# Optimization experiments

Measured on AMD Instinct MI355X. Metric: run time of the kernel, lower is better.

The kernel has to match this reference:

```python
import jax, jax.numpy as jnp
import numpy as np

B, XDIM, TWIN, INCH = 1024, 62, 10, 128
MID, OUT, K, K1, LIN, HC = 256, 512, 3, 10, 512, 4
EPS = 1e-5

REGIONS = [
    list(range(0, 5)),
    list(range(5, 8)) + list(range(14, 17)),
    list(range(8, 11)) + list(range(17, 20)),
    list(range(11, 14)) + list(range(20, 23)),
    list(range(23, 26)) + list(range(32, 35)),
    list(range(26, 29)) + list(range(35, 38)),
    list(range(29, 32)) + list(range(38, 41)),
    list(range(41, 44)) + list(range(50, 52)) + list(range(57, 58)),
    list(range(44, 47)) + list(range(52, 55)) + list(range(58, 61)),
    list(range(47, 50)) + list(range(55, 57)) + list(range(61, 62)),
]


def setup_inputs() -> dict:
    key = jax.random.key(0)
    ks = jax.random.split(key, 40)
    n = lambda k, s, sc=0.02: jax.random.normal(k, s, jnp.float32) * sc
    inp = {
        "x": jax.random.normal(ks[0], (B, XDIM, TWIN, INCH), jnp.float32),
        "tfe_w": n(ks[1], (XDIM, TWIN)),          # depthwise Conv2d (10,1) weight, squeezed
        "tfe_b": jnp.zeros((XDIM,), jnp.float32),
        "cheby1_w": n(ks[2], (K, INCH, OUT)),
        "A": n(ks[3], (XDIM, XDIM)),
        "cheby2_w": n(ks[4], (K, MID, OUT)),
        "A1": n(ks[5], (K1, K1)),
        "b_gate": jnp.float32(1.0),
        "c_gate": jnp.float32(1.0),
        "region_b": jnp.zeros((K1, MID), jnp.float32),
        "hc_w1": n(ks[6], (OUT * 72, LIN)),
        "hc_b1": jnp.zeros((LIN,), jnp.float32),
        "bn1_g": jnp.ones((LIN,), jnp.float32),
        "bn1_b": jnp.zeros((LIN,), jnp.float32),
        "hc_w2": n(ks[7], (LIN, LIN // 2)),
        "hc_b2": jnp.zeros((LIN // 2,), jnp.float32),
        "bn2_g": jnp.ones((LIN // 2,), jnp.float32),
        "bn2_b": jnp.zeros((LIN // 2,), jnp.float32),
        "hc_w3": n(ks[8], (LIN // 2, HC)),
        "hc_b3": jnp.zeros((HC,), jnp.float32),
    }
    for i, idx in enumerate(REGIONS):
        inp[f"rw{i+1}"] = n(ks[10 + i], (MID, INCH, len(idx)))
    return inp


def _cheby(x, L, Ws):
    # sum_k  S_k @ x @ W_k  with S_0 = I, S_k = S_{k-1} @ L ; then ReLU
    S = jnp.eye(L.shape[0], dtype=x.dtype)
    res = jnp.zeros(x.shape[:2] + (Ws.shape[-1],), x.dtype)
    for k in range(Ws.shape[0]):
        res = res + jnp.einsum("nm,bmt,to->bno", S, x, Ws[k])
        S = S @ L
    return jax.nn.relu(res)


def _bn(h, g, b):
    mu = h.mean(axis=0)
    v = h.var(axis=0)  # biased, training-mode BatchNorm1d
    return (h - mu) * jax.lax.rsqrt(v + EPS) * g + b


def _forward(x, tfe_w, tfe_b, cheby1_w, A, cheby2_w, A1, b_gate, c_gate,
             rw1, rw2, rw3, rw4, rw5, rw6, rw7, rw8, rw9, rw10, region_b,
             hc_w1, hc_b1, bn1_g, bn1_b, hc_w2, hc_b2, bn2_g, bn2_b, hc_w3, hc_b3):
    # variance gate (torch.var default: unbiased)
    sigma = jnp.var(x, axis=2, ddof=1)                              # (B, 62, INCH)
    g_tfe = jnp.einsum("bcit,ci->bct", x, tfe_w) + tfe_b[None, :, None]
    g = g_tfe * jnp.exp(-sigma)                                      # (B, 62, INCH)

    g1 = _cheby(g, A, cheby1_w)                                      # (B, 62, OUT)

    rws = [rw1, rw2, rw3, rw4, rw5, rw6, rw7, rw8, rw9, rw10]
    RG = []
    for i, (idx, w) in enumerate(zip(REGIONS, rws)):
        reg = g[:, jnp.asarray(idx), :]                              # (B, L, INCH)
        RG.append(jnp.einsum("blc,mcl->bm", reg, w) + region_b[i])   # Conv1d, full-width kernel
    g2in = jnp.stack(RG, axis=1)                                     # (B, 10, MID)
    g2 = _cheby(g2in, A1, cheby2_w)                                  # (B, 10, OUT)

    att = jnp.concatenate([b_gate * g1, c_gate * g2], axis=1)        # (B, 72, OUT)
    cat = jnp.concatenate([g1, g2], axis=1)
    out = jax.nn.softmax(att, axis=1) * cat
    out = out.reshape(out.shape[0], -1)                              # (B, 72*OUT)

    h = jax.nn.gelu(_bn(out @ hc_w1 + hc_b1, bn1_g, bn1_b), approximate=False)
    h = jax.nn.gelu(_bn(h @ hc_w2 + hc_b2, bn2_g, bn2_b), approximate=False)
    h = h @ hc_w3 + hc_b3
    return jax.nn.softmax(h, axis=1)


def reference(x, tfe_w, tfe_b, cheby1_w, A, cheby2_w, A1, b_gate, c_gate,
              rw1, rw2, rw3, rw4, rw5, rw6, rw7, rw8, rw9, rw10, region_b,
              hc_w1, hc_b1, bn1_g, bn1_b, hc_w2, hc_b2, bn2_g, bn2_b, hc_w3, hc_b3):
    return _forward(x, tfe_w, tfe_b, cheby1_w, A, cheby2_w, A1, b_gate, c_gate,
                    rw1, rw2, rw3, rw4, rw5, rw6, rw7, rw8, rw9, rw10, region_b,
                    hc_w1, hc_b1, bn1_g, bn1_b, hc_w2, hc_b2, bn2_g, bn2_b, hc_w3, hc_b3)
```

## Files before the change

kernel.cpp:

```cpp
#include <hip/hip_runtime.h>
#include <math.h>


__constant__ int cOrder[62] = {
  0,1,2,3,4,
  5,6,7,14,15,16,
  8,9,10,17,18,19,
  11,12,13,20,21,22,
  23,24,25,32,33,34,
  26,27,28,35,36,37,
  29,30,31,38,39,40,
  41,42,43,50,51,57,
  44,45,46,52,53,54,58,59,60,
  47,48,49,55,56,61
};
__constant__ int cPos[62] = {
  0,1,2,3,4, 5,6,7, 11,12,13, 17,18,19, 8,9,10, 14,15,16, 20,21,22,
  23,24,25, 29,30,31, 35,36,37, 26,27,28, 32,33,34, 38,39,40,
  41,42,43, 47,48,49, 56,57,58, 44,45, 50,51,52, 59,60, 46, 53,54,55, 61
};
__constant__ int cRegK[10]   = {640,768,768,768,768,768,768,768,1152,768};
__constant__ int cRegCum[10] = {0,640,1408,2176,2944,3712,4480,5248,6016,7168};

struct Ptr10 { const float* p[10]; };

typedef __attribute__((ext_vector_type(8))) short bf16x8;
typedef __attribute__((ext_vector_type(4))) float f32x4;

__device__ __forceinline__ float gelu_exact(float v){
  return 0.5f * v * (1.0f + erff(v * 0.70710678118654752f));
}
__device__ __forceinline__ unsigned short f2bf(float f){
  unsigned u = __float_as_uint(f);
  unsigned r = (u + 0x7fffu + ((u >> 16) & 1u)) >> 16;
  return (unsigned short)r;
}
__device__ __forceinline__ float bf2f(unsigned short u){
  return __uint_as_float(((unsigned)u) << 16);
}
__device__ __forceinline__ void load_lds16(const unsigned short* g, unsigned short* l){
  __builtin_amdgcn_global_load_lds(
      (const __attribute__((address_space(1))) void*)g,
      (__attribute__((address_space(3))) void*)l, 16, 0, 0);
}

template<bool RELU>
__global__ __launch_bounds__(256) void k_mfma(
    const unsigned short* __restrict__ A, long lda,
    const unsigned short* __restrict__ BT, long ldb,
    void* __restrict__ Cv, int ldc, int kPerZ, long cStrideZ, int mcCount){
  __shared__ unsigned short As[128*32];
  __shared__ unsigned short Bs[128*32];
  int mt, nt, zt;
  if (mcCount){
    int id = blockIdx.x;
    int c = ((id >> 6) << 3) + (id & 7);
    int member = (id >> 3) & 7;
    zt = c / mcCount;
    int mc = c - zt*mcCount;
    mt = mc*2 + (member >> 2);
    nt = member & 3;
  } else { mt = blockIdx.x; nt = blockIdx.y; zt = blockIdx.z; }
  int tid = threadIdx.x;
  int wave = tid >> 6, lane = tid & 63;
  int m0 = mt * 128, n0 = nt * 128;
  int kStart = zt * kPerZ;
  int waveM = wave >> 1, waveN = wave & 1;
  int lr = lane >> 2, ch = lane & 3;
  int quad = lane >> 4, mrow = lane & 15;
  int swe = ((quad ^ (mrow & 3)) << 3);

  int rA0 = wave*32 + lr;
  int rA1 = rA0 + 16;
  int ce  = ((ch ^ (rA0 & 3)) << 3);
  const unsigned short* gA0 = A  + (long)(m0 + rA0)*lda + kStart + ce;
  const unsigned short* gA1 = A  + (long)(m0 + rA1)*lda + kStart + ce;
  const unsigned short* gB0 = BT + (long)(n0 + rA0)*ldb + kStart + ce;
  const unsigned short* gB1 = BT + (long)(n0 + rA1)*ldb + kStart + ce;
  unsigned short* lA0 = &As[(wave*32)*32];
  unsigned short* lA1 = &As[(wave*32+16)*32];
  unsigned short* lB0 = &Bs[(wave*32)*32];
  unsigned short* lB1 = &Bs[(wave*32+16)*32];

  f32x4 acc[4][4] = {};
  int nIter = kPerZ >> 5;
  for (int it = 0; it < nIter; ++it){
    long ko = (long)it << 5;
    load_lds16(gA0 + ko, lA0);
    load_lds16(gA1 + ko, lA1);
    load_lds16(gB0 + ko, lB0);
    load_lds16(gB1 + ko, lB1);
    __syncthreads();
    bf16x8 af[4], bfr[4];
#pragma unroll
    for (int mi = 0; mi < 4; mi++)
      af[mi] = *(const bf16x8*)&As[(waveM*64 + mi*16 + mrow)*32 + swe];
#pragma unroll
    for (int ni = 0; ni < 4; ni++)
      bfr[ni] = *(const bf16x8*)&Bs[(waveN*64 + ni*16 + mrow)*32 + swe];
#pragma unroll
    for (int mi = 0; mi < 4; mi++)
#pragma unroll
      for (int ni = 0; ni < 4; ni++)
        acc[mi][ni] = __builtin_amdgcn_mfma_f32_16x16x32_bf16(
            af[mi], bfr[ni], acc[mi][ni], 0, 0, 0);
    __syncthreads();
  }
  if (RELU){
    unsigned short* C = (unsigned short*)Cv;
#pragma unroll
    for (int mi = 0; mi < 4; mi++)
#pragma unroll
      for (int ni = 0; ni < 4; ni++){
        int col = n0 + waveN*64 + ni*16 + mrow;
#pragma unroll
        for (int r = 0; r < 4; r++){
          int row = m0 + waveM*64 + mi*16 + quad*4 + r;
          C[(long)row*ldc + col] = f2bf(fmaxf(acc[mi][ni][r], 0.f));
        }
      }
  } else {
    float* C = (float*)Cv + (long)zt * cStrideZ;
#pragma unroll
    for (int mi = 0; mi < 4; mi++)
#pragma unroll
      for (int ni = 0; ni < 4; ni++){
        int col = n0 + waveN*64 + ni*16 + mrow;
#pragma unroll
        for (int r = 0; r < 4; r++){
          int row = m0 + waveM*64 + mi*16 + quad*4 + r;
          C[(long)row*ldc + col] = acc[mi][ni][r];
        }
      }
  }
}
template __global__ void k_mfma<true>(const unsigned short*, long, const unsigned short*, long, void*, int, int, long, int);
template __global__ void k_mfma<false>(const unsigned short*, long, const unsigned short*, long, void*, int, int, long, int);

__global__ __launch_bounds__(256) void k_dual(
    const unsigned short* __restrict__ A2c, const unsigned short* __restrict__ B2c,
    unsigned short* __restrict__ C2c,
    const unsigned short* __restrict__ A1c, const unsigned short* __restrict__ B1c,
    unsigned short* __restrict__ C1c){
  __shared__ unsigned short As[128*32];
  __shared__ unsigned short Bs[128*32];
  int id = blockIdx.x;
  bool is1 = id >= 320;
  const unsigned short* A  = is1 ? A1c : A2c;
  const unsigned short* BT = is1 ? B1c : B2c;
  unsigned short* C = is1 ? C1c : C2c;
  long lda = is1 ? 384 : 768;
  long ldb = lda;
  int kPerZ = (int)lda;
  if (is1) id -= 320;
  int c = ((id >> 6) << 3) + (id & 7);
  int member = (id >> 3) & 7;
  int mt = c*2 + (member >> 2);
  int nt = member & 3;
  int tid = threadIdx.x;
  int wave = tid >> 6, lane = tid & 63;
  int m0 = mt * 128, n0 = nt * 128;
  int waveM = wave >> 1, waveN = wave & 1;
  int lr = lane >> 2, ch = lane & 3;
  int quad = lane >> 4, mrow = lane & 15;
  int swe = ((quad ^ (mrow & 3)) << 3);

  int rA0 = wave*32 + lr;
  int rA1 = rA0 + 16;
  int ce  = ((ch ^ (rA0 & 3)) << 3);
  const unsigned short* gA0 = A  + (long)(m0 + rA0)*lda + ce;
  const unsigned short* gA1 = A  + (long)(m0 + rA1)*lda + ce;
  const unsigned short* gB0 = BT + (long)(n0 + rA0)*ldb + ce;
  const unsigned short* gB1 = BT + (long)(n0 + rA1)*ldb + ce;
  unsigned short* lA0 = &As[(wave*32)*32];
  unsigned short* lA1 = &As[(wave*32+16)*32];
  unsigned short* lB0 = &Bs[(wave*32)*32];
  unsigned short* lB1 = &Bs[(wave*32+16)*32];

  f32x4 acc[4][4] = {};
  int nIter = kPerZ >> 5;
  for (int it = 0; it < nIter; ++it){
    long ko = (long)it << 5;
    load_lds16(gA0 + ko, lA0);
    load_lds16(gA1 + ko, lA1);
    load_lds16(gB0 + ko, lB0);
    load_lds16(gB1 + ko, lB1);
    __syncthreads();
    bf16x8 af[4], bfr[4];
#pragma unroll
    for (int mi = 0; mi < 4; mi++)
      af[mi] = *(const bf16x8*)&As[(waveM*64 + mi*16 + mrow)*32 + swe];
#pragma unroll
    for (int ni = 0; ni < 4; ni++)
      bfr[ni] = *(const bf16x8*)&Bs[(waveN*64 + ni*16 + mrow)*32 + swe];
#pragma unroll
    for (int mi = 0; mi < 4; mi++)
#pragma unroll
      for (int ni = 0; ni < 4; ni++)
        acc[mi][ni] = __builtin_amdgcn_mfma_f32_16x16x32_bf16(
            af[mi], bfr[ni], acc[mi][ni], 0, 0, 0);
    __syncthreads();
  }
#pragma unroll
  for (int mi = 0; mi < 4; mi++)
#pragma unroll
    for (int ni = 0; ni < 4; ni++){
      int col = n0 + waveN*64 + ni*16 + mrow;
#pragma unroll
      for (int r = 0; r < 4; r++){
        int row = m0 + waveM*64 + mi*16 + quad*4 + r;
        C[(long)row*512 + col] = f2bf(fmaxf(acc[mi][ni][r], 0.f));
      }
    }
}

__global__ __launch_bounds__(256) void k_mid(
    const unsigned short* __restrict__ ARb, const float* __restrict__ AT,
    const float* __restrict__ A2T, unsigned short* __restrict__ xcat,
    const unsigned short* __restrict__ RWT, const float* __restrict__ regb,
    float* __restrict__ g2in){
  __shared__ __align__(16) char smraw[32768];
  int id = blockIdx.x;
  int tid = threadIdx.x;
  if (id < 1024){
    float* sgn = (float*)smraw;
    int b = id;
    for (int i = tid; i < 7936; i += 256){
      int p = i >> 7, c = i & 127;
      sgn[cOrder[p]*128 + c] = bf2f(ARb[(long)b*7936 + i]);
    }
    __syncthreads();
    int c = tid & 127, mat = tid >> 7;
    const float* MT = mat ? A2T : AT;
    float acc[62];
#pragma unroll
    for (int n = 0; n < 62; n++) acc[n] = 0.f;
    for (int m = 0; m < 62; m++){
      float gv = sgn[m*128 + c];
      const float* Mp = MT + m*62;
#pragma unroll
      for (int n = 0; n < 62; n++) acc[n] = fmaf(Mp[n], gv, acc[n]);
    }
    long base = (long)b*23808 + (mat+1)*128 + c;
#pragma unroll
    for (int n = 0; n < 62; n++) xcat[base + (long)n*384] = f2bf(acc[n]);
    return;
  }
  unsigned short* As = (unsigned short*)smraw;
  unsigned short* Bs = As + 128*32;
  int id2 = id - 1024;
  int z = id2 >> 4;
  int m  = id2 & 15;
  int mt = m >> 1, nt = m & 1;
  int K = cRegK[z];
  int cumk = cRegCum[z];
  const unsigned short* A  = ARb + cumk;
  const unsigned short* BT = RWT + (long)cumk*256;
  long lda = 7936, ldb = K;
  int wave = tid >> 6, lane = tid & 63;
  int m0 = mt * 128, n0 = nt * 128;
  int waveM = wave >> 1, waveN = wave & 1;
  int lr = lane >> 2, ch = lane & 3;
  int quad = lane >> 4, mrow = lane & 15;
  int swe = ((quad ^ (mrow & 3)) << 3);

  int rA0 = wave*32 + lr;
  int rA1 = rA0 + 16;
  int ce  = ((ch ^ (rA0 & 3)) << 3);
  const unsigned short* gA0 = A  + (long)(m0 + rA0)*lda + ce;
  const unsigned short* gA1 = A  + (long)(m0 + rA1)*lda + ce;
  const unsigned short* gB0 = BT + (long)(n0 + rA0)*ldb + ce;
  const unsigned short* gB1 = BT + (long)(n0 + rA1)*ldb + ce;
  unsigned short* lA0 = &As[(wave*32)*32];
  unsigned short* lA1 = &As[(wave*32+16)*32];
  unsigned short* lB0 = &Bs[(wave*32)*32];
  unsigned short* lB1 = &Bs[(wave*32+16)*32];

  f32x4 acc[4][4] = {};
  int nIter = K >> 5;
  for (int it = 0; it < nIter; ++it){
    long ko = (long)it << 5;
    load_lds16(gA0 + ko, lA0);
    load_lds16(gA1 + ko, lA1);
    load_lds16(gB0 + ko, lB0);
    load_lds16(gB1 + ko, lB1);
    __syncthreads();
    bf16x8 af[4], bfr[4];
#pragma unroll
    for (int mi = 0; mi < 4; mi++)
      af[mi] = *(const bf16x8*)&As[(waveM*64 + mi*16 + mrow)*32 + swe];
#pragma unroll
    for (int ni = 0; ni < 4; ni++)
      bfr[ni] = *(const bf16x8*)&Bs[(waveN*64 + ni*16 + mrow)*32 + swe];
#pragma unroll
    for (int mi = 0; mi < 4; mi++)
#pragma unroll
      for (int ni = 0; ni < 4; ni++)
        acc[mi][ni] = __builtin_amdgcn_mfma_f32_16x16x32_bf16(
            af[mi], bfr[ni], acc[mi][ni], 0, 0, 0);
    __syncthreads();
  }
#pragma unroll
  for (int mi = 0; mi < 4; mi++)
#pragma unroll
    for (int ni = 0; ni < 4; ni++){
      int col = n0 + waveN*64 + ni*16 + mrow;
      float bias = regb[z*256 + col];
#pragma unroll
      for (int r = 0; r < 4; r++){
        int row = m0 + waveM*64 + mi*16 + quad*4 + r;
        g2in[(long)row*2560 + z*256 + col] = acc[mi][ni][r] + bias;
      }
    }
}

__global__ __launch_bounds__(256) void k_front(
    const float* __restrict__ s0, unsigned short* __restrict__ d0,
    const float* __restrict__ s1, unsigned short* __restrict__ d1,
    const float* __restrict__ s2, unsigned short* __restrict__ d2,
    const float* __restrict__ s3, unsigned short* __restrict__ d3,
    Ptr10 rws, unsigned short* __restrict__ RWT,
    const float* __restrict__ Amat, float* __restrict__ AT,
    float* __restrict__ A2T,
    const float* __restrict__ x, const float* __restrict__ tw,
    const float* __restrict__ tb, unsigned short* __restrict__ arb,
    unsigned short* __restrict__ xcat, float* __restrict__ sumz){
  __shared__ float smem[64*65];
  int id = blockIdx.x;
  int tid = threadIdx.x;
  if (id >= 15342){
    *(float4*)(sumz + (id-15342)*1024 + tid*4) = make_float4(0.f,0.f,0.f,0.f);
    return;
  }
  if (id >= 7406){
    int q = id - 7406;
    int r = tid >> 5, j = tid & 31;
    int idx = q*8 + r;
    int b = idx / 62, n = idx - b*62;
    const float4* xp = (const float4*)(x + (long)idx*1280) + j;
    float sx=0.f,sy=0.f,sz=0.f,sw=0.f;
    float qx=0.f,qy=0.f,qz=0.f,qw=0.f;
    float gx=0.f,gy=0.f,gz=0.f,gw=0.f;
#pragma unroll
    for (int i = 0; i < 10; i++){
      float4 v = xp[i*32];
      float w = tw[n*10+i];
      sx+=v.x; sy+=v.y; sz+=v.z; sw+=v.w;
      qx=fmaf(v.x,v.x,qx); qy=fmaf(v.y,v.y,qy);
      qz=fmaf(v.z,v.z,qz); qw=fmaf(v.w,v.w,qw);
      gx=fmaf(v.x,w,gx); gy=fmaf(v.y,w,gy);
      gz=fmaf(v.z,w,gz); gw=fmaf(v.w,w,gw);
    }
    float tbn = tb[n];
    float mx_=sx*0.1f, my_=sy*0.1f, mz_=sz*0.1f, mw_=sw*0.1f;
    float rx = (gx+tbn)*expf(-(qx-10.f*mx_*mx_)*(1.f/9.f));
    float ry = (gy+tbn)*expf(-(qy-10.f*my_*my_)*(1.f/9.f));
    float rz = (gz+tbn)*expf(-(qz-10.f*mz_*mz_)*(1.f/9.f));
    float rw = (gw+tbn)*expf(-(qw-10.f*mw_*mw_)*(1.f/9.f));
    ushort4 u = make_ushort4(f2bf(rx), f2bf(ry), f2bf(rz), f2bf(rw));
    *(ushort4*)(arb  + (long)b*7936  + cPos[n]*128 + j*4) = u;
    *(ushort4*)(xcat + (long)b*23808 + n*384       + j*4) = u;
    return;
  }
  if (id < 7344 && id >= 4784){
    int q = id - 4784;
    int z = q >> 8, m = q & 255;
    int K = cRegK[z], L = K >> 7;
    const float* rw = rws.p[z] + (long)m*K;
    unsigned short* dst = RWT + (long)cRegCum[z]*256 + (long)m*K;
    for (int i = tid; i < K; i += 256) smem[i] = rw[i];
    __syncthreads();
    for (int k = tid; k < K; k += 256){
      int l = k >> 7, c = k & 127;
      dst[k] = f2bf(smem[c*L + l]);
    }
    return;
  }
  if (id >= 7344){
    int r = id - 7344, c = tid;
    if (c < 62) smem[c] = Amat[r*62 + c];
    __syncthreads();
    if (c < 62){
      AT[c*62 + r] = smem[c];
      float s = 0.f;
      for (int t = 0; t < 62; t++) s = fmaf(smem[t], Amat[t*62 + c], s);
      A2T[c*62 + r] = s;
    }
    return;
  }
  const float* src; unsigned short* dst; int R, C, rt, ct;
  if (id < 4608){ src=s0; dst=d0; R=36864; C=512; rt=id>>3;  ct=id&7; }
  else if (id < 4640){ int q=id-4608; src=s1; dst=d1; R=512; C=256; rt=q>>2; ct=q&3; }
  else if (id < 4688){ int q=id-4640; src=s2; dst=d2; R=384; C=512; rt=q>>3; ct=q&7; }
  else { int q=id-4688; src=s3; dst=d3; R=768; C=512; rt=q>>3; ct=q&7; }
  int r0 = rt*64, c0 = ct*64;
  int rr = tid >> 2, cb = (tid & 3) << 2;
#pragma unroll
  for (int i = 0; i < 4; i++){
    int cc = cb + i*16;
    float4 v = *(const float4*)(src + (long)(r0+rr)*C + c0 + cc);
    smem[rr*65+cc+0]=v.x; smem[rr*65+cc+1]=v.y;
    smem[rr*65+cc+2]=v.z; smem[rr*65+cc+3]=v.w;
  }
  __syncthreads();
  int cc = tid >> 2, rb = (tid & 3) << 2;
#pragma unroll
  for (int i = 0; i < 4; i++){
    int r = rb + i*16;
    ushort4 u = make_ushort4(f2bf(smem[(r+0)*65+cc]), f2bf(smem[(r+1)*65+cc]),
                             f2bf(smem[(r+2)*65+cc]), f2bf(smem[(r+3)*65+cc]));
    *(ushort4*)(dst + (long)(c0+cc)*R + r0 + r) = u;
  }
}

__global__ __launch_bounds__(256) void k_x2cat(
    const float* __restrict__ g2in, const float* __restrict__ A1,
    unsigned short* __restrict__ X2){
  __shared__ float sg[2560];
  __shared__ float sA1[100];
  __shared__ float sA2[100];
  int b = blockIdx.x, tid = threadIdx.x;
  for (int i = tid; i < 2560; i += 256) sg[i] = g2in[(long)b*2560 + i];
  if (tid < 100) sA1[tid] = A1[tid];
  __syncthreads();
  if (tid < 100){
    int n = tid/10, m = tid - n*10;
    float a = 0.f;
#pragma unroll
    for (int t = 0; t < 10; t++) a = fmaf(sA1[n*10+t], sA1[t*10+m], a);
    sA2[tid] = a;
  }
  __syncthreads();
  for (int i = tid; i < 2560; i += 256){
    int n = i >> 8, t = i & 255;
    float v1 = 0.f, v2 = 0.f;
#pragma unroll
    for (int m = 0; m < 10; m++){
      float gv = sg[(m<<8) + t];
      v1 = fmaf(sA1[n*10+m], gv, v1);
      v2 = fmaf(sA2[n*10+m], gv, v2);
    }
    long base = (long)b*7680 + n*768;
    X2[base + t]       = f2bf(sg[i]);
    X2[base + 256 + t] = f2bf(v1);
    X2[base + 512 + t] = f2bf(v2);
  }
}

__global__ __launch_bounds__(256) void k_softcat(
    const unsigned short* __restrict__ g1, const unsigned short* __restrict__ g2,
    const float* __restrict__ bg_, const float* __restrict__ cg_,
    unsigned short* __restrict__ outb){
  int b = blockIdx.x;
  int o = blockIdx.y*256 + threadIdx.x;
  float v[72];
  const unsigned short* p1 = g1 + (long)b*62*512 + o;
#pragma unroll
  for (int j = 0; j < 62; j++) v[j] = bf2f(p1[j*512]);
  const unsigned short* p2 = g2 + (long)b*10*512 + o;
#pragma unroll
  for (int j = 0; j < 10; j++) v[62+j] = bf2f(p2[j*512]);
  float bg = *bg_, cg = *cg_;
  float mx = -1e30f;
#pragma unroll
  for (int j = 0; j < 72; j++){
    float av = (j < 62 ? bg : cg) * v[j];
    mx = fmaxf(mx, av);
  }
  float sum = 0.f;
#pragma unroll
  for (int j = 0; j < 72; j++){
    float e = expf((j < 62 ? bg : cg) * v[j] - mx);
    sum += e;
    v[j] = e * v[j];
  }
  float inv = 1.f / sum;
  unsigned short* op = outb + (long)b*36864 + o;
#pragma unroll
  for (int j = 0; j < 72; j++) op[j*512] = f2bf(v[j] * inv);
}

__global__ __launch_bounds__(256) void k_tail1(
    const float4* __restrict__ P, const float* __restrict__ gam,
    const float* __restrict__ bet, float* __restrict__ sum,
    float* __restrict__ ssq, unsigned int* __restrict__ cnt,
    unsigned short* __restrict__ h1b){
  __shared__ float4 ls[128], ls2[128];
  int tid = threadIdx.x;
  int c  = tid & 127;
  int rr = tid >> 7;
  int r0 = blockIdx.x * 8;
  float4 va[4];
  float4 s1 = make_float4(0.f,0.f,0.f,0.f);
  float4 s2 = make_float4(0.f,0.f,0.f,0.f);
#pragma unroll
  for (int k = 0; k < 4; k++){
    int row = r0 + rr + 2*k;
    long idx = (long)row*128 + c;
    float4 v = make_float4(0.f,0.f,0.f,0.f);
#pragma unroll
    for (int s = 0; s < 16; s++){
      float4 p = P[(long)s*131072 + idx];
      v.x += p.x; v.y += p.y; v.z += p.z; v.w += p.w;
    }
    va[k] = v;
    s1.x += v.x; s1.y += v.y; s1.z += v.z; s1.w += v.w;
    s2.x = fmaf(v.x,v.x,s2.x); s2.y = fmaf(v.y,v.y,s2.y);
    s2.z = fmaf(v.z,v.z,s2.z); s2.w = fmaf(v.w,v.w,s2.w);
  }
  if (rr){ ls[c] = s1; ls2[c] = s2; }
  __syncthreads();
  if (!rr){
    float4 o1 = ls[c], o2 = ls2[c];
    atomicAdd(&sum[c*4+0], s1.x+o1.x); atomicAdd(&sum[c*4+1], s1.y+o1.y);
    atomicAdd(&sum[c*4+2], s1.z+o1.z); atomicAdd(&sum[c*4+3], s1.w+o1.w);
    atomicAdd(&ssq[c*4+0], s2.x+o2.x); atomicAdd(&ssq[c*4+1], s2.y+o2.y);
    atomicAdd(&ssq[c*4+2], s2.z+o2.z); atomicAdd(&ssq[c*4+3], s2.w+o2.w);
  }
  __threadfence();
  __syncthreads();
  if (tid == 0){
    __hip_atomic_fetch_add(cnt, 1u, __ATOMIC_RELEASE, __HIP_MEMORY_SCOPE_AGENT);
    while (__hip_atomic_load(cnt, __ATOMIC_ACQUIRE, __HIP_MEMORY_SCOPE_AGENT) < 128u)
      __builtin_amdgcn_s_sleep(16);
  }
  __syncthreads();
  int j = c*4;
  float mu0 = __hip_atomic_load(&sum[j+0], __ATOMIC_RELAXED, __HIP_MEMORY_SCOPE_AGENT)*(1.f/1024.f);
  float mu1 = __hip_atomic_load(&sum[j+1], __ATOMIC_RELAXED, __HIP_MEMORY_SCOPE_AGENT)*(1.f/1024.f);
  float mu2 = __hip_atomic_load(&sum[j+2], __ATOMIC_RELAXED, __HIP_MEMORY_SCOPE_AGENT)*(1.f/1024.f);
  float mu3 = __hip_atomic_load(&sum[j+3], __ATOMIC_RELAXED, __HIP_MEMORY_SCOPE_AGENT)*(1.f/1024.f);
  float q0 = __hip_atomic_load(&ssq[j+0], __ATOMIC_RELAXED, __HIP_MEMORY_SCOPE_AGENT);
  float q1 = __hip_atomic_load(&ssq[j+1], __ATOMIC_RELAXED, __HIP_MEMORY_SCOPE_AGENT);
  float q2 = __hip_atomic_load(&ssq[j+2], __ATOMIC_RELAXED, __HIP_MEMORY_SCOPE_AGENT);
  float q3 = __hip_atomic_load(&ssq[j+3], __ATOMIC_RELAXED, __HIP_MEMORY_SCOPE_AGENT);
  float rs0 = rsqrtf(q0*(1.f/1024.f) - mu0*mu0 + 1e-5f);
  float rs1 = rsqrtf(q1*(1.f/1024.f) - mu1*mu1 + 1e-5f);
  float rs2 = rsqrtf(q2*(1.f/1024.f) - mu2*mu2 + 1e-5f);
  float rs3 = rsqrtf(q3*(1.f/1024.f) - mu3*mu3 + 1e-5f);
  float g0 = gam[j+0], g1 = gam[j+1], g2 = gam[j+2], g3 = gam[j+3];
  float b0 = bet[j+0], b1 = bet[j+1], b2 = bet[j+2], b3 = bet[j+3];
#pragma unroll
  for (int k = 0; k < 4; k++){
    int row = r0 + rr + 2*k;
    float4 v = va[k];
    ushort4 u;
    u.x = f2bf(gelu_exact((v.x - mu0)*rs0*g0 + b0));
    u.y = f2bf(gelu_exact((v.y - mu1)*rs1*g1 + b1));
    u.z = f2bf(gelu_exact((v.z - mu2)*rs2*g2 + b2));
    u.w = f2bf(gelu_exact((v.w - mu3)*rs3*g3 + b3));
    *(ushort4*)(h1b + (long)row*512 + j) = u;
  }
}

__global__ __launch_bounds__(256) void k_tail2(
    const float* __restrict__ P2, const float* __restrict__ gam,
    const float* __restrict__ bet, const float* __restrict__ w3,
    const float* __restrict__ b3, float* __restrict__ sum,
    float* __restrict__ ssq, unsigned int* __restrict__ cnt,
    float* __restrict__ outp){
  __shared__ float lv[32][257];
  __shared__ float rd[32][8][4];
  int tid = threadIdx.x;
  int rbase = blockIdx.x * 32;
  float v[32];
  float s = 0.f, s2 = 0.f;
#pragma unroll 8
  for (int r = 0; r < 32; r++){
    int row = rbase + r;
    float a = 0.f;
#pragma unroll
    for (int sp = 0; sp < 4; sp++)
      a += P2[((long)sp*1024 + row)*256 + tid];
    v[r] = a;
    s += a; s2 = fmaf(a, a, s2);
  }
  atomicAdd(&sum[tid], s);
  atomicAdd(&ssq[tid], s2);
  __threadfence();
  __syncthreads();
  if (tid == 0){
    __hip_atomic_fetch_add(cnt, 1u, __ATOMIC_RELEASE, __HIP_MEMORY_SCOPE_AGENT);
    while (__hip_atomic_load(cnt, __ATOMIC_ACQUIRE, __HIP_MEMORY_SCOPE_AGENT) < 32u)
      __builtin_amdgcn_s_sleep(16);
  }
  __syncthreads();
  float mu = __hip_atomic_load(&sum[tid], __ATOMIC_RELAXED, __HIP_MEMORY_SCOPE_AGENT)*(1.f/1024.f);
  float qq = __hip_atomic_load(&ssq[tid], __ATOMIC_RELAXED, __HIP_MEMORY_SCOPE_AGENT);
  float rs = rsqrtf(qq*(1.f/1024.f) - mu*mu + 1e-5f);
  float gm = gam[tid], bt = bet[tid];
#pragma unroll 8
  for (int r = 0; r < 32; r++)
    lv[r][tid] = gelu_exact((v[r] - mu)*rs*gm + bt);
  __syncthreads();
  int row = tid >> 3, seg = tid & 7;
  float p0=0.f,p1=0.f,p2=0.f,p3=0.f;
#pragma unroll
  for (int i = 0; i < 32; i++){
    int cc = seg*32 + i;
    float a = lv[row][cc];
    float4 w = ((const float4*)w3)[cc];
    p0 = fmaf(a, w.x, p0); p1 = fmaf(a, w.y, p1);
    p2 = fmaf(a, w.z, p2); p3 = fmaf(a, w.w, p3);
  }
  rd[row][seg][0]=p0; rd[row][seg][1]=p1; rd[row][seg][2]=p2; rd[row][seg][3]=p3;
  __syncthreads();
  if (tid < 32){
    float l[4];
#pragma unroll
    for (int c = 0; c < 4; c++){
      float a = 0.f;
#pragma unroll
      for (int g = 0; g < 8; g++) a += rd[tid][g][c];
      l[c] = a + b3[c];
    }
    float m = fmaxf(fmaxf(l[0], l[1]), fmaxf(l[2], l[3]));
    float e[4]; float su = 0.f;
#pragma unroll
    for (int c = 0; c < 4; c++){ e[c] = expf(l[c]-m); su += e[c]; }
    float inv = 1.f / su;
#pragma unroll
    for (int c = 0; c < 4; c++) outp[(long)(rbase+tid)*4 + c] = e[c]*inv;
  }
}

extern "C" void kernel_launch(void* const* d_in, const int* in_sizes, int n_in,
                              void* d_out, int out_size, void* d_ws, size_t ws_size,
                              hipStream_t stream){
  (void)n_in; (void)out_size; (void)ws_size;
  bool dictOrder = (in_sizes[9] == 2560);
  const float* x     = (const float*)d_in[0];
  const float* tfe_w = (const float*)d_in[1];
  const float* tfe_b = (const float*)d_in[2];
  const float* ch1w  = (const float*)d_in[3];
  const float* Amat  = (const float*)d_in[4];
  const float* ch2w  = (const float*)d_in[5];
  const float* A1mat = (const float*)d_in[6];
  const float* bgate = (const float*)d_in[7];
  const float* cgate = (const float*)d_in[8];
  const float* regb  = (const float*)d_in[dictOrder ? 9 : 19];
  int o = dictOrder ? 0 : 10;
  const float* hc_w1 = (const float*)d_in[10+o];
  const float* bn1g  = (const float*)d_in[12+o];
  const float* bn1b  = (const float*)d_in[13+o];
  const float* hc_w2 = (const float*)d_in[14+o];
  const float* bn2g  = (const float*)d_in[16+o];
  const float* bn2b  = (const float*)d_in[17+o];
  const float* hc_w3 = (const float*)d_in[18+o];
  const float* hc_b3 = (const float*)d_in[19+o];
  Ptr10 rws;
  for (int i = 0; i < 10; i++) rws.p[i] = (const float*)d_in[(dictOrder ? 20 : 9) + i];

  char* Wb = (char*)d_ws;
  unsigned short* ARb   = (unsigned short*)(Wb + 0);
  unsigned short* XCAT  = (unsigned short*)(Wb + 16252928);
  unsigned short* RWT   = (unsigned short*)(Wb + 65011712);
  float*          G2IN  = (float*)(Wb + 69074944);
  unsigned short* X2CAT = (unsigned short*)(Wb + 79560704);
  unsigned short* W1T   = (unsigned short*)(Wb + 95289344);
  unsigned short* WC1T  = (unsigned short*)(Wb + 133038080);
  unsigned short* WC2T  = (unsigned short*)(Wb + 133431296);
  unsigned short* G1    = (unsigned short*)(Wb + 134217728);
  unsigned short* G2    = (unsigned short*)(Wb + 199229440);
  unsigned short* OUTB  = (unsigned short*)(Wb + 0);
  float*          P     = (float*)(Wb + 209715200);
  float*          SUM1  = (float*)(Wb + 246415360);
  float*          SSQ1  = SUM1 + 512;
  float*          SUM2  = SUM1 + 1024;
  float*          SSQ2  = SUM1 + 1280;
  unsigned int*   CNT1  = (unsigned int*)(SUM1 + 1536);
  unsigned int*   CNT2  = (unsigned int*)(SUM1 + 1537);
  float*          AT    = (float*)(Wb + 246423552);
  float*          A2T   = (float*)(Wb + 246439040);
  unsigned short* W2T   = (unsigned short*)(Wb + 246454528);
  unsigned short* H1B   = (unsigned short*)(Wb + 246716928);

  k_front<<<15344, 256, 0, stream>>>(hc_w1, W1T, hc_w2, W2T, ch1w, WC1T,
                                     ch2w, WC2T, rws, RWT, Amat, AT, A2T,
                                     x, tfe_w, tfe_b, ARb, XCAT, SUM1);
  k_mid<<<1184, 256, 0, stream>>>(ARb, AT, A2T, XCAT, RWT, regb, G2IN);
  k_x2cat<<<1024, 256, 0, stream>>>(G2IN, A1mat, X2CAT);
  k_dual<<<2304, 256, 0, stream>>>(X2CAT, WC2T, G2, XCAT, WC1T, G1);
  k_softcat<<<dim3(1024,2), 256, 0, stream>>>(G1, G2, bgate, cgate, OUTB);
  k_mfma<false><<<512, 256, 0, stream>>>(OUTB, 36864, W1T, 36864, (void*)P, 512, 2304, 524288, 4);
  k_tail1<<<128, 256, 0, stream>>>((const float4*)P, bn1g, bn1b, SUM1, SSQ1, CNT1, H1B);
  k_mfma<false><<<dim3(8,2,4), 256, 0, stream>>>(H1B, 512, W2T, 512, (void*)P, 256, 128, 262144, 0);
  k_tail2<<<32, 256, 0, stream>>>(P, bn2g, bn2b, hc_w3, hc_b3, SUM2, SSQ2, CNT2, (float*)d_out);
}
```

Before: 883.1 us.

## Compute graph propagation A·x and A²·x with bf16 MFMA in k_mid

The per-batch graph propagation in k_mid (multiplying the 62-node signal by A and A², stored transposed) previously ran as scalar fp32 FMAs with 62 accumulators per thread. It now uses bf16 MFMA 16x16x32 tiles on swizzled LDS copies of the signal and of zero-padded 64x64 bf16 A and A² matrices, which k_front produces. This cuts per-thread register pressure and ALU work, at the cost of rounding A and A² to bf16 and some padding waste.

```diff
diff --git a/kernel.cpp b/kernel.cpp
--- a/kernel.cpp
+++ b/kernel.cpp
@@ -215,35 +215,72 @@
 }
 
 __global__ __launch_bounds__(256) void k_mid(
-    const unsigned short* __restrict__ ARb, const float* __restrict__ AT,
-    const float* __restrict__ A2T, unsigned short* __restrict__ xcat,
+    const unsigned short* __restrict__ ARb, const unsigned short* __restrict__ Ab,
+    const unsigned short* __restrict__ A2b, unsigned short* __restrict__ xcat,
     const unsigned short* __restrict__ RWT, const float* __restrict__ regb,
     float* __restrict__ g2in){
   __shared__ __align__(16) char smraw[32768];
   int id = blockIdx.x;
   int tid = threadIdx.x;
   if (id < 1024){
-    float* sgn = (float*)smraw;
+    unsigned short* gT  = (unsigned short*)smraw;
+    unsigned short* AbL = gT + 128*64;
     int b = id;
+    const unsigned short* arp = ARb + (long)b*7936;
     for (int i = tid; i < 7936; i += 256){
       int p = i >> 7, c = i & 127;
-      sgn[cOrder[p]*128 + c] = bf2f(ARb[(long)b*7936 + i]);
-    }
-    __syncthreads();
-    int c = tid & 127, mat = tid >> 7;
-    const float* MT = mat ? A2T : AT;
-    float acc[62];
-#pragma unroll
-    for (int n = 0; n < 62; n++) acc[n] = 0.f;
-    for (int m = 0; m < 62; m++){
-      float gv = sgn[m*128 + c];
-      const float* Mp = MT + m*62;
-#pragma unroll
-      for (int n = 0; n < 62; n++) acc[n] = fmaf(Mp[n], gv, acc[n]);
-    }
-    long base = (long)b*23808 + (mat+1)*128 + c;
-#pragma unroll
-    for (int n = 0; n < 62; n++) xcat[base + (long)n*384] = f2bf(acc[n]);
+      int m = cOrder[p];
+      gT[(c<<6) + (((m>>3) ^ (c&7))<<3) + (m&7)] = arp[i];
+    }
+    {
+      int c = tid >> 1, m = 62 + (tid & 1);
+      gT[(c<<6) + ((7 ^ (c&7))<<3) + (m&7)] = 0;
+    }
+    for (int q = tid; q < 1024; q += 256){
+      int mm = q >> 9, qq = q & 511;
+      int row = qq >> 3, ch = qq & 7;
+      const unsigned short* src = mm ? A2b : Ab;
+      *(bf16x8*)&AbL[mm*4096 + (row<<6) + ((ch ^ (row&7))<<3)] =
+        *(const bf16x8*)&src[(row<<6) + (ch<<3)];
+    }
+    __syncthreads();
+    int wave = tid >> 6, lane = tid & 63;
+    int quad = lane >> 4, mrow = lane & 15;
+    int mat = wave >> 1, wc = wave & 1;
+    const unsigned short* Am = AbL + mat*4096;
+    f32x4 acc[4][4] = {};
+#pragma unroll
+    for (int s = 0; s < 2; s++){
+      bf16x8 af[4], bfr[4];
+#pragma unroll
+      for (int mi = 0; mi < 4; mi++){
+        int row = mi*16 + mrow;
+        af[mi] = *(const bf16x8*)&Am[(row<<6) + ((((s<<2)|quad) ^ (row&7))<<3)];
+      }
+#pragma unroll
+      for (int ni = 0; ni < 4; ni++){
+        int row = wc*64 + ni*16 + mrow;
+        bfr[ni] = *(const bf16x8*)&gT[(row<<6) + ((((s<<2)|quad) ^ (row&7))<<3)];
+      }
+#pragma unroll
+      for (int mi = 0; mi < 4; mi++)
+#pragma unroll
+        for (int ni = 0; ni < 4; ni++)
+          acc[mi][ni] = __builtin_amdgcn_mfma_f32_16x16x32_bf16(
+              af[mi], bfr[ni], acc[mi][ni], 0, 0, 0);
+    }
+    long xb = (long)b*23808 + (mat+1)*128;
+#pragma unroll
+    for (int mi = 0; mi < 4; mi++)
+#pragma unroll
+      for (int ni = 0; ni < 4; ni++){
+        int c = wc*64 + ni*16 + mrow;
+#pragma unroll
+        for (int r = 0; r < 4; r++){
+          int n = mi*16 + quad*4 + r;
+          if (n < 62) xcat[xb + (long)n*384 + c] = f2bf(acc[mi][ni][r]);
+        }
+      }
     return;
   }
   unsigned short* As = (unsigned short*)smraw;
@@ -320,8 +357,8 @@
     const float* __restrict__ s2, unsigned short* __restrict__ d2,
     const float* __restrict__ s3, unsigned short* __restrict__ d3,
     Ptr10 rws, unsigned short* __restrict__ RWT,
-    const float* __restrict__ Amat, float* __restrict__ AT,
-    float* __restrict__ A2T,
+    const float* __restrict__ Amat, unsigned short* __restrict__ AbW,
+    unsigned short* __restrict__ A2bW,
     const float* __restrict__ x, const float* __restrict__ tw,
     const float* __restrict__ tb, unsigned short* __restrict__ arb,
     unsigned short* __restrict__ xcat, float* __restrict__ sumz){
@@ -380,11 +417,22 @@
     int r = id - 7344, c = tid;
     if (c < 62) smem[c] = Amat[r*62 + c];
     __syncthreads();
-    if (c < 62){
-      AT[c*62 + r] = smem[c];
-      float s = 0.f;
-      for (int t = 0; t < 62; t++) s = fmaf(smem[t], Amat[t*62 + c], s);
-      A2T[c*62 + r] = s;
+    if (c < 64){
+      unsigned short av = 0, a2v = 0;
+      if (c < 62){
+        av = f2bf(smem[c]);
+        float s = 0.f;
+        for (int t = 0; t < 62; t++) s = fmaf(smem[t], Amat[t*62 + c], s);
+        a2v = f2bf(s);
+      }
+      AbW [r*64 + c] = av;
+      A2bW[r*64 + c] = a2v;
+    }
+    if (r == 0 && c >= 64 && c < 192){
+      int q = c - 64;
+      int rr = 62 + (q >> 6), cc = q & 63;
+      AbW [rr*64 + cc] = 0;
+      A2bW[rr*64 + cc] = 0;
     }
     return;
   }
@@ -670,15 +718,15 @@
   float*          SSQ2  = SUM1 + 1280;
   unsigned int*   CNT1  = (unsigned int*)(SUM1 + 1536);
   unsigned int*   CNT2  = (unsigned int*)(SUM1 + 1537);
-  float*          AT    = (float*)(Wb + 246423552);
-  float*          A2T   = (float*)(Wb + 246439040);
+  unsigned short* Ab    = (unsigned short*)(Wb + 246423552);
+  unsigned short* A2b   = (unsigned short*)(Wb + 246439040);
   unsigned short* W2T   = (unsigned short*)(Wb + 246454528);
   unsigned short* H1B   = (unsigned short*)(Wb + 246716928);
 
   k_front<<<15344, 256, 0, stream>>>(hc_w1, W1T, hc_w2, W2T, ch1w, WC1T,
-                                     ch2w, WC2T, rws, RWT, Amat, AT, A2T,
+                                     ch2w, WC2T, rws, RWT, Amat, Ab, A2b,
                                      x, tfe_w, tfe_b, ARb, XCAT, SUM1);
-  k_mid<<<1184, 256, 0, stream>>>(ARb, AT, A2T, XCAT, RWT, regb, G2IN);
+  k_mid<<<1184, 256, 0, stream>>>(ARb, Ab, A2b, XCAT, RWT, regb, G2IN);
   k_x2cat<<<1024, 256, 0, stream>>>(G2IN, A1mat, X2CAT);
   k_dual<<<2304, 256, 0, stream>>>(X2CAT, WC2T, G2, XCAT, WC1T, G1);
   k_softcat<<<dim3(1024,2), 256, 0, stream>>>(G1, G2, bgate, cgate, OUTB);
```

Result: faster. 811.9 us (-8.1%).
